# Optimization experiments

Hardware: AMD Instinct MI355X
Metric: run time of the kernel (lower is better)

The kernel has to match this reference:

```python
import jax, jax.numpy as jnp
import numpy as np

B, S, D, C, H, E, K, L = 32, 512, 768, 3072, 1024, 8, 2, 2


def _layernorm(x, g, b, eps=1e-5):
    mu = jnp.mean(x, axis=-1, keepdims=True)
    var = jnp.var(x, axis=-1, keepdims=True)
    return (x - mu) * jax.lax.rsqrt(var + eps) * g + b


def setup_inputs() -> dict:
    key = jax.random.key(0)
    ks = jax.random.split(key, 12)
    s = 0.02
    return {
        "hidden_states": jax.random.normal(ks[0], (B, S, C), jnp.float32),
        "proj_w": jax.random.normal(ks[1], (C, D), jnp.float32) * s,
        "proj_b": jnp.zeros((D,), jnp.float32),
        "ln1_g": jnp.ones((D,), jnp.float32),
        "ln1_b": jnp.zeros((D,), jnp.float32),
        "gate_w": jax.random.normal(ks[2], (D, E), jnp.float32) * s,
        "gate_b": jnp.zeros((E,), jnp.float32),
        "w1": jax.random.normal(ks[3], (E, D, H), jnp.float32) * s,
        "b1": jnp.zeros((E, H), jnp.float32),
        "w2": jax.random.normal(ks[4], (E, H, D), jnp.float32) * s,
        "b2": jnp.zeros((E, D), jnp.float32),
        "ln2_g": jnp.ones((D,), jnp.float32),
        "ln2_b": jnp.zeros((D,), jnp.float32),
        "cls_w": jax.random.normal(ks[5], (D, L), jnp.float32) * s,
        "cls_b": jnp.zeros((L,), jnp.float32),
    }


def reference(hidden_states, proj_w, proj_b, ln1_g, ln1_b, gate_w, gate_b,
              w1, b1, w2, b2, ln2_g, ln2_b, cls_w, cls_b):
    # layer_projection: Linear -> LayerNorm -> GELU (dropout = identity in eval)
    x = jnp.einsum('bsc,cd->bsd', hidden_states, proj_w) + proj_b
    x = _layernorm(x, ln1_g, ln1_b)
    seq_out = jax.nn.gelu(x, approximate=False)  # [B,S,D]

    # Router: gate -> softmax -> top-k -> renormalize
    probs = jax.nn.softmax(seq_out @ gate_w + gate_b, axis=-1)  # [B,S,E]
    top_w, top_i = jax.lax.top_k(probs, K)                      # [B,S,K]
    top_w = top_w / jnp.sum(top_w, axis=-1, keepdims=True)

    # combine[t,e] = sum_k top_w[t,k] * (top_i[t,k]==e)
    combine = jnp.sum(jax.nn.one_hot(top_i, E, dtype=top_w.dtype)
                      * top_w[..., None], axis=-2)              # [B,S,E]

    xt = seq_out.reshape(-1, D)                                 # [T,D]
    ct = combine.reshape(-1, E)                                 # [T,E]
    h = jax.nn.gelu(jnp.einsum('td,edh->eth', xt, w1) + b1[:, None, :],
                    approximate=False)                          # [E,T,H]
    eo = jnp.einsum('eth,ehd->etd', h, w2) + b2[:, None, :]     # [E,T,D]
    moe = jnp.einsum('etd,te->td', eo, ct).reshape(B, S, D)

    moe = _layernorm(moe + seq_out, ln2_g, ln2_b)
    logits = moe @ cls_w + cls_b                                # [B,S,2]
    return logits
```

## Files before the change

kernel.cpp:

```cpp
#include <hip/hip_runtime.h>
#include <hip/hip_bf16.h>

#define T_TOK 16384
#define CDIM 3072
#define DDIM 768
#define HDIM 1024
#define NEXP 8
#define NSLOT 33792
#define MAXTILE 264
#define AMB_CAP 2048
#define AMB2_CAP 256
#define KSPLIT 4
#define NSEG 8

typedef __attribute__((ext_vector_type(8))) short bfrag;
typedef __attribute__((ext_vector_type(4))) float f32x4;
typedef __attribute__((ext_vector_type(4))) float fvec4;

__device__ __forceinline__ unsigned short bf16_rn(float f) {
  union { float f; unsigned u; } v; v.f = f;
  unsigned r = v.u + 0x7fffu + ((v.u >> 16) & 1u);
  return (unsigned short)(r >> 16);
}
__device__ __forceinline__ float bf16_f32(unsigned short h) {
  union { unsigned u; float f; } v; v.u = ((unsigned)h) << 16;
  return v.f;
}
__device__ __forceinline__ float gelu_exact(float x) {
  return 0.5f * x * (1.0f + erff(x * 0.70710678118654752440f));
}
__device__ __forceinline__ void glds16(const void* g, void* l) {
  __builtin_amdgcn_global_load_lds((const __attribute__((address_space(1))) void*)g,
                                   (__attribute__((address_space(3))) void*)l, 16, 0, 0);
}

__global__ void k_init(int* token_list, int* counts, int* cursors, unsigned short* zero_row,
                       int* amb_count, int* amb2_count) {
  int i = blockIdx.x * 256 + threadIdx.x;
  for (int j = i; j < NSLOT; j += 64 * 256) token_list[j] = -1;
  if (i < NEXP) counts[i] = 0;
  if (i < 128) cursors[i] = 0;
  if (i == 0) { *amb_count = 0; *amb2_count = 0; }
  if (i < 1024) zero_row[i] = 0;
}

__global__ void k_cast_tiled(const float* __restrict__ src,
                             unsigned short* __restrict__ dst) {
  __shared__ unsigned short h[128][136];
  int rb = blockIdx.x;
  int cc = blockIdx.y;
  int tid = threadIdx.x;
  const float* in = src + ((size_t)rb * 128) * CDIM + cc * 128;
#pragma unroll
  for (int it = 0; it < 16; ++it) {
    int idx = it * 256 + tid;
    int r = idx >> 5, nv = idx & 31;
    fvec4 v = *(const fvec4*)(in + (size_t)r * CDIM + nv * 4);
    unsigned long long p = (unsigned long long)bf16_rn(v[0]) |
                           ((unsigned long long)bf16_rn(v[1]) << 16) |
                           ((unsigned long long)bf16_rn(v[2]) << 32) |
                           ((unsigned long long)bf16_rn(v[3]) << 48);
    *(unsigned long long*)&h[r][nv * 4] = p;
  }
  __syncthreads();
  unsigned short* ob = dst + ((size_t)rb * 96 + cc * 4) * 4096;
#pragma unroll
  for (int kt = 0; kt < 4; ++kt) {
#pragma unroll
    for (int it = 0; it < 2; ++it) {
      int gg = it * 256 + tid;
      int kg = gg >> 7, r = gg & 127;
      bfrag o = *(const bfrag*)&h[r][kt * 32 + kg * 8];
      *(bfrag*)(ob + ((size_t)kt * 512 + gg) * 8) = o;
    }
  }
}

__global__ void k_transpose_split(const float* __restrict__ src,
                                  unsigned short* __restrict__ dhi,
                                  unsigned short* __restrict__ dlo) {
  __shared__ unsigned short h[128][72], l[128][72];
  int nb2 = blockIdx.x;
  int cb = blockIdx.y;
  int col_blk = nb2 >> 1, nhalf = nb2 & 1;
  int n0 = col_blk * 128 + nhalf * 64;
  int tid = threadIdx.x;
  const float* in = src + (size_t)(cb * 128) * DDIM + n0;
#pragma unroll
  for (int it = 0; it < 8; ++it) {
    int idx = it * 256 + tid;
    int cl = idx >> 4, nv = idx & 15;
    fvec4 v = *(const fvec4*)(in + (size_t)cl * DDIM + nv * 4);
    unsigned long long ph = 0, pl = 0;
#pragma unroll
    for (int e = 0; e < 4; ++e) {
      unsigned short hh = bf16_rn(v[e]);
      unsigned short ll = bf16_rn(v[e] - bf16_f32(hh));
      ph |= (unsigned long long)hh << (16 * e);
      pl |= (unsigned long long)ll << (16 * e);
    }
    *(unsigned long long*)&h[cl][nv * 4] = ph;
    *(unsigned long long*)&l[cl][nv * 4] = pl;
  }
  __syncthreads();
  size_t obase = ((size_t)col_blk * 96 + cb * 4) * 4096;
#pragma unroll
  for (int kt = 0; kt < 4; ++kt) {
    int kg = tid >> 6, rl = tid & 63;
    bfrag oh, ol;
#pragma unroll
    for (int e = 0; e < 8; ++e) {
      int c = kt * 32 + kg * 8 + e;
      oh[e] = (short)h[c][rl];
      ol[e] = (short)l[c][rl];
    }
    size_t gi = obase + ((size_t)kt * 512 + kg * 128 + nhalf * 64 + rl) * 8;
    *(bfrag*)(dhi + gi) = oh;
    *(bfrag*)(dlo + gi) = ol;
  }
}

__global__ void k_transpose_tiled(const float* __restrict__ src0,
                                  unsigned short* __restrict__ dst0, int K, int N) {
  __shared__ unsigned short h[128][72];
  int nb2 = blockIdx.x;
  int cb = blockIdx.y;
  int z = blockIdx.z;
  int col_blk = nb2 >> 1, nhalf = nb2 & 1;
  int n0 = col_blk * 128 + nhalf * 64;
  int tid = threadIdx.x;
  const float* in = src0 + (size_t)z * K * N + (size_t)(cb * 128) * N + n0;
#pragma unroll
  for (int it = 0; it < 8; ++it) {
    int idx = it * 256 + tid;
    int cl = idx >> 4, nv = idx & 15;
    fvec4 v = *(const fvec4*)(in + (size_t)cl * N + nv * 4);
    unsigned long long ph = 0;
#pragma unroll
    for (int e = 0; e < 4; ++e)
      ph |= (unsigned long long)bf16_rn(v[e]) << (16 * e);
    *(unsigned long long*)&h[cl][nv * 4] = ph;
  }
  __syncthreads();
  size_t obase = (size_t)z * K * N + ((size_t)col_blk * (K / 32) + cb * 4) * 4096;
#pragma unroll
  for (int kt = 0; kt < 4; ++kt) {
    int kg = tid >> 6, rl = tid & 63;
    bfrag oh;
#pragma unroll
    for (int e = 0; e < 8; ++e) oh[e] = (short)h[kt * 32 + kg * 8 + e][rl];
    *(bfrag*)(dst0 + obase + ((size_t)kt * 512 + kg * 128 + nhalf * 64 + rl) * 8) = oh;
  }
}

__launch_bounds__(256, 3)
__global__ void k_gemm1(const unsigned short* __restrict__ Atil,
                        const unsigned short* __restrict__ Btil,
                        float* __restrict__ Cout)
{
  __shared__ unsigned short sA[12288], sB[12288];
  int tid = threadIdx.x;
  int lane = tid & 63, wave = tid >> 6;
  int id = blockIdx.x;
  int swz = (id & 7) * 96 + (id >> 3);
  int brow = swz / 6, bcol = swz % 6;
  int row0 = brow * 128, col0 = bcol * 128;
  int wm = wave >> 1, wn = wave & 1;

  f32x4 acc[4][4];
#pragma unroll
  for (int i = 0; i < 4; ++i)
#pragma unroll
    for (int j = 0; j < 4; ++j) acc[i][j] = (f32x4){0.f, 0.f, 0.f, 0.f};

  int rsel = lane & 15, kq = lane >> 4;
  const unsigned short* At = Atil + (size_t)(brow * 96) * 4096;
  const unsigned short* Bt = Btil + (size_t)(bcol * 96) * 4096;

  auto STAGE = [&](int kt, int b) {
    const unsigned short* as = At + (size_t)kt * 4096;
    const unsigned short* bs = Bt + (size_t)kt * 4096;
    int lbase = b * 4096;
#pragma unroll
    for (int pass = 0; pass < 2; ++pass) {
      int g = pass * 256 + tid;
      int li = lbase + (pass * 256 + wave * 64) * 8;
      glds16(as + (size_t)g * 8, &sA[li]);
      glds16(bs + (size_t)g * 8, &sB[li]);
    }
  };

  STAGE(0, 0);
  STAGE(1, 1);
  int b0 = 0;
  for (int kt = 0; kt < 96; ++kt) {
    if (kt < 95) asm volatile("s_waitcnt vmcnt(4)" ::: "memory");
    else         asm volatile("s_waitcnt vmcnt(0)" ::: "memory");
    __builtin_amdgcn_s_barrier();
    if (kt + 2 < 96) {
      int bn = b0 + 2; if (bn >= 3) bn -= 3;
      STAGE(kt + 2, bn);
    }
    int lb = b0 * 4096;
    bfrag af[4], bf[4];
#pragma unroll
    for (int i = 0; i < 4; ++i) {
      af[i] = *(const bfrag*)&sA[lb + (kq * 128 + wm * 64 + i * 16 + rsel) * 8];
      bf[i] = *(const bfrag*)&sB[lb + (kq * 128 + wn * 64 + i * 16 + rsel) * 8];
    }
#pragma unroll
    for (int i = 0; i < 4; ++i)
#pragma unroll
      for (int j = 0; j < 4; ++j)
        acc[i][j] = __builtin_amdgcn_mfma_f32_16x16x32_bf16(af[i], bf[j], acc[i][j], 0, 0, 0);
    b0 = (b0 == 2) ? 0 : b0 + 1;
  }

  int cc = lane & 15, rr = (lane >> 4) * 4;
#pragma unroll
  for (int i = 0; i < 4; ++i)
#pragma unroll
    for (int j = 0; j < 4; ++j)
#pragma unroll
      for (int r = 0; r < 4; ++r) {
        int row = row0 + wm * 64 + i * 16 + rr + r;
        int col = col0 + wn * 64 + j * 16 + cc;
        Cout[(size_t)row * DDIM + col] = acc[i][j][r];
      }
}

__launch_bounds__(256)
__global__ void k_ln_router(const float* __restrict__ xw, const float* __restrict__ proj_b,
                            const float* __restrict__ g1, const float* __restrict__ b1v,
                            const float* __restrict__ gate_w, const float* __restrict__ gate_b,
                            unsigned short* __restrict__ seq_b16,
                            int* __restrict__ top_i, float* __restrict__ top_w,
                            int* __restrict__ amb_list, int* __restrict__ amb_count)
{
  int lane = threadIdx.x & 63;
  int t = blockIdx.x * 4 + (threadIdx.x >> 6);
  const float* xr = xw + (size_t)t * DDIM;
  float x0[12];
  float s = 0.f, s2 = 0.f;
#pragma unroll
  for (int j = 0; j < 12; ++j) {
    int d = lane + 64 * j;
    float v = xr[d] + proj_b[d];
    x0[j] = v; s += v; s2 += v * v;
  }
#pragma unroll
  for (int o = 32; o > 0; o >>= 1) { s += __shfl_xor(s, o, 64); s2 += __shfl_xor(s2, o, 64); }
  float mu = s * (1.f / DDIM);
  float rstd = rsqrtf(s2 * (1.f / DDIM) - mu * mu + 1e-5f);
  float acc8[8];
#pragma unroll
  for (int e = 0; e < 8; ++e) acc8[e] = 0.f;
#pragma unroll
  for (int j = 0; j < 12; ++j) {
    int d = lane + 64 * j;
    float y = (x0[j] - mu) * rstd * g1[d] + b1v[d];
    float ge = gelu_exact(y);
    seq_b16[(size_t)t * DDIM + d] = bf16_rn(ge);
    const float* gw = gate_w + (size_t)d * NEXP;
#pragma unroll
    for (int e = 0; e < 8; ++e) acc8[e] += ge * gw[e];
  }
#pragma unroll
  for (int e = 0; e < 8; ++e)
#pragma unroll
    for (int o = 32; o > 0; o >>= 1) acc8[e] += __shfl_xor(acc8[e], o, 64);
  if (lane == 0) {
    float lg[8];
#pragma unroll
    for (int e = 0; e < 8; ++e) lg[e] = acc8[e] + gate_b[e];
    int i0 = 0;
    for (int e = 1; e < 8; ++e) if (lg[e] > lg[i0]) i0 = e;
    int i1 = (i0 == 0) ? 1 : 0;
    for (int e = 0; e < 8; ++e) if (e != i0 && lg[e] > lg[i1]) i1 = e;
    float l2 = -1e30f;
    for (int e = 0; e < 8; ++e) if (e != i0 && e != i1 && lg[e] > l2) l2 = lg[e];
    if (lg[i1] - l2 < 8e-3f) {
      int p = atomicAdd(amb_count, 1);
      if (p < AMB_CAP) amb_list[p] = t;
    }
    float w0 = 1.f / (1.f + expf(lg[i1] - lg[i0]));
    top_i[t * 2] = i0; top_i[t * 2 + 1] = i1;
    top_w[t * 2] = w0; top_w[t * 2 + 1] = 1.f - w0;
  }
}

__launch_bounds__(256, 2)
__global__ void k_repair(const float* __restrict__ hidden,
                         const unsigned short* __restrict__ BTh,
                         const unsigned short* __restrict__ BTl,
                         const int* __restrict__ amb_list, const int* __restrict__ amb_count,
                         float* __restrict__ xw_fix4)
{
  int n = *amb_count; if (n > AMB_CAP) n = AMB_CAP;
  int by = blockIdx.y;
  if (by * 128 >= n) return;
  int bx = blockIdx.x;
  int z = blockIdx.z;
  int col0 = bx * 128;
  __shared__ unsigned short sAh[8192], sAl[8192], sBh[8192], sBl[8192];
  __shared__ int tk[128];
  int tid = threadIdx.x, lane = tid & 63, wave = tid >> 6;
  if (tid < 128) tk[tid] = (by * 128 + tid < n) ? amb_list[by * 128 + tid] : -1;
  __syncthreads();
  int wm = wave >> 1, wn = wave & 1;
  f32x4 acc[4][4];
#pragma unroll
  for (int i = 0; i < 4; ++i)
#pragma unroll
    for (int j = 0; j < 4; ++j) acc[i][j] = (f32x4){0.f, 0.f, 0.f, 0.f};
  int rsel = lane & 15, kq = lane >> 4;
  int ktbase = z * 24;
  const unsigned short* Bth = BTh + (size_t)(bx * 96) * 4096;
  const unsigned short* Btl = BTl + (size_t)(bx * 96) * 4096;

  auto STAGE = [&](int kt, int b) {
    int k0 = (ktbase + kt) * 32;
    int lb = b * 4096;
    size_t tb = (size_t)(ktbase + kt) * 4096;
#pragma unroll
    for (int pass = 0; pass < 2; ++pass) {
      int g = pass * 256 + tid;
      int kg = g >> 7, r = g & 127;
      int tok = tk[r];
      fvec4 a0 = (fvec4){0.f, 0.f, 0.f, 0.f}, a1 = a0;
      if (tok >= 0) {
        const float* ap = hidden + (size_t)tok * CDIM + k0 + kg * 8;
        a0 = *(const fvec4*)ap;
        a1 = *(const fvec4*)(ap + 4);
      }
      bfrag hv, lv;
#pragma unroll
      for (int u = 0; u < 8; ++u) {
        float v = (u < 4) ? a0[u] : a1[u - 4];
        unsigned short h = bf16_rn(v);
        hv[u] = (short)h;
        lv[u] = (short)bf16_rn(v - bf16_f32(h));
      }
      *(bfrag*)&sAh[lb + (size_t)g * 8] = hv;
      *(bfrag*)&sAl[lb + (size_t)g * 8] = lv;
      int li = lb + (pass * 256 + wave * 64) * 8;
      glds16(Bth + tb + (size_t)g * 8, &sBh[li]);
      glds16(Btl + tb + (size_t)g * 8, &sBl[li]);
    }
  };

  STAGE(0, 0);
  __syncthreads();
  for (int kt = 0; kt < 24; ++kt) {
    int b = kt & 1;
    if (kt + 1 < 24) STAGE(kt + 1, b ^ 1);
    int lb = b * 4096;
    bfrag ah[4], al[4], bh[4], bl[4];
#pragma unroll
    for (int i = 0; i < 4; ++i) {
      int ra = wm * 64 + i * 16 + rsel;
      ah[i] = *(const bfrag*)&sAh[lb + (kq * 128 + ra) * 8];
      al[i] = *(const bfrag*)&sAl[lb + (kq * 128 + ra) * 8];
      int cb = wn * 64 + i * 16 + rsel;
      bh[i] = *(const bfrag*)&sBh[lb + (kq * 128 + cb) * 8];
      bl[i] = *(const bfrag*)&sBl[lb + (kq * 128 + cb) * 8];
    }
#pragma unroll
    for (int i = 0; i < 4; ++i)
#pragma unroll
      for (int j = 0; j < 4; ++j) {
        acc[i][j] = __builtin_amdgcn_mfma_f32_16x16x32_bf16(ah[i], bh[j], acc[i][j], 0, 0, 0);
        acc[i][j] = __builtin_amdgcn_mfma_f32_16x16x32_bf16(ah[i], bl[j], acc[i][j], 0, 0, 0);
        acc[i][j] = __builtin_amdgcn_mfma_f32_16x16x32_bf16(al[i], bh[j], acc[i][j], 0, 0, 0);
      }
    __syncthreads();
  }
  float* dst = xw_fix4 + (size_t)z * AMB_CAP * DDIM;
  int cc = lane & 15, rr = (lane >> 4) * 4;
#pragma unroll
  for (int i = 0; i < 4; ++i)
#pragma unroll
    for (int j = 0; j < 4; ++j)
#pragma unroll
      for (int r = 0; r < 4; ++r) {
        int row = by * 128 + wm * 64 + i * 16 + rr + r;
        int col = col0 + wn * 64 + j * 16 + cc;
        dst[(size_t)row * DDIM + col] = acc[i][j][r];
      }
}

__launch_bounds__(256)
__global__ void k_fix2(const float* __restrict__ xw_fix4, const float* __restrict__ proj_b,
                       const float* __restrict__ g1, const float* __restrict__ b1v,
                       const float* __restrict__ gate_w, const float* __restrict__ gate_b,
                       const int* __restrict__ amb_list, const int* __restrict__ amb_count,
                       int* __restrict__ top_i, float* __restrict__ top_w,
                       int* __restrict__ amb2_list, int* __restrict__ amb2_count)
{
  int n = *amb_count; if (n > AMB_CAP) n = AMB_CAP;
  int lane = threadIdx.x & 63;
  int slot = blockIdx.x * 4 + (threadIdx.x >> 6);
  if (slot >= n) return;
  int t = amb_list[slot];
  const float* p0 = xw_fix4 + (size_t)slot * DDIM;
  const float* p1 = p0 + (size_t)AMB_CAP * DDIM;
  const float* p2 = p1 + (size_t)AMB_CAP * DDIM;
  const float* p3 = p2 + (size_t)AMB_CAP * DDIM;
  float x0[12];
  float s = 0.f, s2 = 0.f;
#pragma unroll
  for (int j = 0; j < 12; ++j) {
    int d = lane + 64 * j;
    float v = ((p0[d] + p1[d]) + (p2[d] + p3[d])) + proj_b[d];
    x0[j] = v; s += v; s2 += v * v;
  }
#pragma unroll
  for (int o = 32; o > 0; o >>= 1) { s += __shfl_xor(s, o, 64); s2 += __shfl_xor(s2, o, 64); }
  float mu = s * (1.f / DDIM);
  float rstd = rsqrtf(s2 * (1.f / DDIM) - mu * mu + 1e-5f);
  float acc8[8];
#pragma unroll
  for (int e = 0; e < 8; ++e) acc8[e] = 0.f;
#pragma unroll
  for (int j = 0; j < 12; ++j) {
    int d = lane + 64 * j;
    float y = (x0[j] - mu) * rstd * g1[d] + b1v[d];
    float ge = gelu_exact(y);
    const float* gw = gate_w + (size_t)d * NEXP;
#pragma unroll
    for (int e = 0; e < 8; ++e) acc8[e] += ge * gw[e];
  }
#pragma unroll
  for (int e = 0; e < 8; ++e)
#pragma unroll
    for (int o = 32; o > 0; o >>= 1) acc8[e] += __shfl_xor(acc8[e], o, 64);
  if (lane == 0) {
    float lg[8];
#pragma unroll
    for (int e = 0; e < 8; ++e) lg[e] = acc8[e] + gate_b[e];
    int i0 = 0;
    for (int e = 1; e < 8; ++e) if (lg[e] > lg[i0]) i0 = e;
    int i1 = (i0 == 0) ? 1 : 0;
    for (int e = 0; e < 8; ++e) if (e != i0 && lg[e] > lg[i1]) i1 = e;
    float l2 = -1e30f;
    for (int e = 0; e < 8; ++e) if (e != i0 && e != i1 && lg[e] > l2) l2 = lg[e];
    if (lg[i1] - l2 < 2e-4f) {
      int p = atomicAdd(amb2_count, 1);
      if (p < AMB2_CAP) amb2_list[p] = t;
    }
    float w0 = 1.f / (1.f + expf(lg[i1] - lg[i0]));
    top_i[t * 2] = i0; top_i[t * 2 + 1] = i1;
    top_w[t * 2] = w0; top_w[t * 2 + 1] = 1.f - w0;
  }
}

__launch_bounds__(256, 1)
__global__ void k_router_fix(const float* __restrict__ hidden, const float* __restrict__ proj_w,
                             const int* __restrict__ amb2_list, const int* __restrict__ amb2_count,
                             double* __restrict__ xpart)
{
  __shared__ float hrow[384];
  int tid = threadIdx.x;
  int seg = blockIdx.y;
  int cbase = seg * 384;
  int n = *amb2_count; if (n > AMB2_CAP) n = AMB2_CAP;
  for (int ii = blockIdx.x; ii < n; ii += gridDim.x) {
    int t = amb2_list[ii];
    __syncthreads();
    if (tid < 96)
      *(fvec4*)&hrow[tid * 4] = *(const fvec4*)(hidden + (size_t)t * CDIM + cbase + tid * 4);
    __syncthreads();
    double p0a = 0.0, p0b = 0.0, p1a = 0.0, p1b = 0.0, p2a = 0.0, p2b = 0.0;
    for (int c0 = 0; c0 < 384; c0 += 16) {
      float w0r[16], w1r[16], w2r[16];
      const float* wp = proj_w + (size_t)(cbase + c0) * DDIM + tid;
#pragma unroll
      for (int u = 0; u < 16; ++u) {
        w0r[u] = wp[u * DDIM];
        w1r[u] = wp[u * DDIM + 256];
        w2r[u] = wp[u * DDIM + 512];
      }
#pragma unroll
      for (int u = 0; u < 16; ++u) {
        double h = (double)hrow[c0 + u];
        if (u & 1) { p0b += h * (double)w0r[u]; p1b += h * (double)w1r[u]; p2b += h * (double)w2r[u]; }
        else       { p0a += h * (double)w0r[u]; p1a += h * (double)w1r[u]; p2a += h * (double)w2r[u]; }
      }
    }
    double* xp = xpart + ((size_t)seg * AMB2_CAP + ii) * DDIM;
    xp[tid] = p0a + p0b;
    xp[tid + 256] = p1a + p1b;
    xp[tid + 512] = p2a + p2b;
  }
}

__launch_bounds__(256)
__global__ void k_fix3(const double* __restrict__ xpart, const float* __restrict__ proj_b,
                       const float* __restrict__ g1, const float* __restrict__ b1v,
                       const float* __restrict__ gate_w, const float* __restrict__ gate_b,
                       const int* __restrict__ amb2_list, const int* __restrict__ amb2_count,
                       int* __restrict__ top_i, float* __restrict__ top_w)
{
  __shared__ double redA[4], redB[4], red8[4][8];
  int n = *amb2_count; if (n > AMB2_CAP) n = AMB2_CAP;
  int ii = blockIdx.x;
  if (ii >= n) return;
  int t = amb2_list[ii];
  int tid = threadIdx.x, lane = tid & 63, wave = tid >> 6;
  double x[3]; double s = 0.0, s2 = 0.0;
#pragma unroll
  for (int j = 0; j < 3; ++j) {
    int d = tid + 256 * j;
    double acc = (double)proj_b[d];
#pragma unroll
    for (int seg = 0; seg < NSEG; ++seg)
      acc += xpart[((size_t)seg * AMB2_CAP + ii) * DDIM + d];
    x[j] = acc; s += acc; s2 += acc * acc;
  }
#pragma unroll
  for (int o = 32; o > 0; o >>= 1) { s += __shfl_down(s, o, 64); s2 += __shfl_down(s2, o, 64); }
  if (lane == 0) { redA[wave] = s; redB[wave] = s2; }
  __syncthreads();
  double mu = (redA[0] + redA[1] + redA[2] + redA[3]) / DDIM;
  double ms = (redB[0] + redB[1] + redB[2] + redB[3]) / DDIM;
  double rstd = 1.0 / sqrt(ms - mu * mu + 1e-5);
  double a8[8];
#pragma unroll
  for (int e = 0; e < 8; ++e) a8[e] = 0.0;
#pragma unroll
  for (int j = 0; j < 3; ++j) {
    int d = tid + 256 * j;
    double y = (x[j] - mu) * rstd * (double)g1[d] + (double)b1v[d];
    double ge = 0.5 * y * (1.0 + erf(y * 0.7071067811865475244));
#pragma unroll
    for (int e = 0; e < 8; ++e) a8[e] += ge * (double)gate_w[(size_t)d * NEXP + e];
  }
#pragma unroll
  for (int e = 0; e < 8; ++e)
#pragma unroll
    for (int o = 32; o > 0; o >>= 1) a8[e] += __shfl_down(a8[e], o, 64);
  if (lane == 0) {
#pragma unroll
    for (int e = 0; e < 8; ++e) red8[wave][e] = a8[e];
  }
  __syncthreads();
  if (tid == 0) {
    double lg[8];
#pragma unroll
    for (int e = 0; e < 8; ++e)
      lg[e] = red8[0][e] + red8[1][e] + red8[2][e] + red8[3][e] + (double)gate_b[e];
    int i0 = 0;
    for (int e = 1; e < 8; ++e) if (lg[e] > lg[i0]) i0 = e;
    int i1 = (i0 == 0) ? 1 : 0;
    for (int e = 0; e < 8; ++e) if (e != i0 && e != i1 && lg[e] > lg[i1]) i1 = e;
    double w0 = 1.0 / (1.0 + exp(lg[i1] - lg[i0]));
    top_i[t * 2] = i0; top_i[t * 2 + 1] = i1;
    top_w[t * 2] = (float)w0; top_w[t * 2 + 1] = (float)(1.0 - w0);
  }
}

__global__ void k_count(const int* __restrict__ top_i, int* __restrict__ counts) {
  __shared__ int h[NEXP];
  int tid = threadIdx.x;
  if (tid < NEXP) h[tid] = 0;
  __syncthreads();
  for (int i = blockIdx.x * 256 + tid; i < 2 * T_TOK; i += 64 * 256)
    atomicAdd(&h[top_i[i]], 1);
  __syncthreads();
  if (tid < NEXP) atomicAdd(&counts[tid], h[tid]);
}

__global__ void k_offsets(const int* __restrict__ counts, int* __restrict__ seg_start,
                          int* __restrict__ padded_total, int* __restrict__ tile_expert) {
  if (threadIdx.x != 0 || blockIdx.x != 0) return;
  int st[NEXP], en[NEXP];
  int s = 0;
  for (int e = 0; e < NEXP; ++e) {
    st[e] = s; seg_start[e] = s;
    s += (counts[e] + 127) & ~127;
    en[e] = s;
  }
  *padded_total = s;
  int nt = s >> 7;
  for (int x = 0; x < nt; ++x) {
    int r = x << 7, e = 0;
    for (int q = 0; q < NEXP; ++q) if (r >= st[q] && r < en[q]) e = q;
    tile_expert[x] = e;
  }
}

__global__ void k_scatter(const int* __restrict__ top_i, const int* __restrict__ seg_start,
                          int* __restrict__ cursors, int* __restrict__ token_list,
                          int* __restrict__ slot_of) {
  __shared__ int lc[NEXP];
  __shared__ int lbase[NEXP];
  int tid = threadIdx.x;
  int t = blockIdx.x * 256 + tid;
  if (tid < NEXP) lc[tid] = 0;
  __syncthreads();
  int e0 = top_i[t * 2], e1 = top_i[t * 2 + 1];
  int o0 = atomicAdd(&lc[e0], 1);
  int o1 = atomicAdd(&lc[e1], 1);
  __syncthreads();
  if (tid < NEXP) lbase[tid] = atomicAdd(&cursors[tid << 4], lc[tid]);
  __syncthreads();
  int p0 = seg_start[e0] + lbase[e0] + o0;
  int p1 = seg_start[e1] + lbase[e1] + o1;
  token_list[p0] = t;
  token_list[p1] = t;
  slot_of[t * 2] = p0;
  slot_of[t * 2 + 1] = p1;
}

__launch_bounds__(256, 4)
__global__ void k_gemm2(const unsigned short* __restrict__ Abase,
                        const unsigned short* __restrict__ w1T,
                        const float* __restrict__ b1,
                        const int* __restrict__ token_list,
                        const int* __restrict__ tile_expert,
                        const int* __restrict__ padded_total,
                        const unsigned short* __restrict__ zero_row,
                        unsigned short* __restrict__ hbuf)
{
  int by = blockIdx.x;
  if (by * 128 >= *padded_total) return;
  int bx = blockIdx.y;
  int e = tile_expert[by];
  __shared__ unsigned short sA[8192], sB[8192];
  __shared__ int tk[128];
  int tid = threadIdx.x, lane = tid & 63, wave = tid >> 6;
  if (tid < 128) tk[tid] = token_list[by * 128 + tid];
  __syncthreads();
  int col0 = bx * 128;
  int wm = wave >> 1, wn = wave & 1;
  f32x4 acc[4][4];
#pragma unroll
  for (int i = 0; i < 4; ++i)
#pragma unroll
    for (int j = 0; j < 4; ++j) acc[i][j] = (f32x4){0.f, 0.f, 0.f, 0.f};
  const unsigned short* Bt = w1T + (size_t)e * HDIM * DDIM + (size_t)bx * (DDIM / 32) * 4096;
  int rsel = lane & 15, kq = lane >> 4;

  auto STAGE = [&](int kt, int b) {
    int k0 = kt * 32;
    int lbase2 = b * 4096;
    size_t tb = (size_t)kt * 4096;
#pragma unroll
    for (int pass = 0; pass < 2; ++pass) {
      int g = pass * 256 + tid;
      int kg = g >> 7, r = g & 127;
      int tok = tk[r];
      const unsigned short* asrc =
          (tok >= 0) ? (Abase + (size_t)tok * DDIM + k0 + kg * 8) : zero_row;
      int li = lbase2 + (pass * 256 + wave * 64) * 8;
      glds16(asrc, &sA[li]);
      glds16(Bt + tb + (size_t)g * 8, &sB[li]);
    }
  };

  STAGE(0, 0);
  __syncthreads();
  for (int kt = 0; kt < 24; ++kt) {
    int b = kt & 1;
    if (kt + 1 < 24) STAGE(kt + 1, b ^ 1);
    int lb = b * 4096;
    bfrag af[4], bf[4];
#pragma unroll
    for (int i = 0; i < 4; ++i) {
      af[i] = *(const bfrag*)&sA[lb + (kq * 128 + wm * 64 + i * 16 + rsel) * 8];
      bf[i] = *(const bfrag*)&sB[lb + (kq * 128 + wn * 64 + i * 16 + rsel) * 8];
    }
#pragma unroll
    for (int i = 0; i < 4; ++i)
#pragma unroll
      for (int j = 0; j < 4; ++j)
        acc[i][j] = __builtin_amdgcn_mfma_f32_16x16x32_bf16(af[i], bf[j], acc[i][j], 0, 0, 0);
    __syncthreads();
  }
  int cc = lane & 15, rr = (lane >> 4) * 4;
#pragma unroll
  for (int i = 0; i < 4; ++i)
#pragma unroll
    for (int j = 0; j < 4; ++j)
#pragma unroll
      for (int r = 0; r < 4; ++r) {
        int row = by * 128 + wm * 64 + i * 16 + rr + r;
        int col = col0 + wn * 64 + j * 16 + cc;
        float x = acc[i][j][r] + b1[(size_t)e * HDIM + col];
        hbuf[(size_t)row * HDIM + col] = bf16_rn(gelu_exact(x));
      }
}

__launch_bounds__(256, 4)
__global__ void k_gemm3(const unsigned short* __restrict__ hbuf,
                        const unsigned short* __restrict__ w2T,
                        const float* __restrict__ b2,
                        const int* __restrict__ tile_expert,
                        const int* __restrict__ padded_total,
                        float* __restrict__ eo)
{
  int by = blockIdx.x;
  if (by * 128 >= *padded_total) return;
  int bx = blockIdx.y;
  int e = tile_expert[by];
  __shared__ unsigned short sA[8192], sB[8192];
  int tid = threadIdx.x, lane = tid & 63, wave = tid >> 6;
  int col0 = bx * 128;
  int wm = wave >> 1, wn = wave & 1;
  f32x4 acc[4][4];
#pragma unroll
  for (int i = 0; i < 4; ++i)
#pragma unroll
    for (int j = 0; j < 4; ++j) acc[i][j] = (f32x4){0.f, 0.f, 0.f, 0.f};
  const unsigned short* Bt = w2T + (size_t)e * DDIM * HDIM + (size_t)bx * (HDIM / 32) * 4096;
  int rsel = lane & 15, kq = lane >> 4;

  auto STAGE = [&](int kt, int b) {
    int k0 = kt * 32;
    int lbase2 = b * 4096;
    size_t tb = (size_t)kt * 4096;
#pragma unroll
    for (int pass = 0; pass < 2; ++pass) {
      int g = pass * 256 + tid;
      int kg = g >> 7, r = g & 127;
      int li = lbase2 + (pass * 256 + wave * 64) * 8;
      glds16(hbuf + (size_t)(by * 128 + r) * HDIM + k0 + kg * 8, &sA[li]);
      glds16(Bt + tb + (size_t)g * 8, &sB[li]);
    }
  };

  STAGE(0, 0);
  __syncthreads();
  for (int kt = 0; kt < 32; ++kt) {
    int b = kt & 1;
    if (kt + 1 < 32) STAGE(kt + 1, b ^ 1);
    int lb = b * 4096;
    bfrag af[4], bf[4];
#pragma unroll
    for (int i = 0; i < 4; ++i) {
      af[i] = *(const bfrag*)&sA[lb + (kq * 128 + wm * 64 + i * 16 + rsel) * 8];
      bf[i] = *(const bfrag*)&sB[lb + (kq * 128 + wn * 64 + i * 16 + rsel) * 8];
    }
#pragma unroll
    for (int i = 0; i < 4; ++i)
#pragma unroll
      for (int j = 0; j < 4; ++j)
        acc[i][j] = __builtin_amdgcn_mfma_f32_16x16x32_bf16(af[i], bf[j], acc[i][j], 0, 0, 0);
    __syncthreads();
  }
  int cc = lane & 15, rr = (lane >> 4) * 4;
#pragma unroll
  for (int i = 0; i < 4; ++i)
#pragma unroll
    for (int j = 0; j < 4; ++j)
#pragma unroll
      for (int r = 0; r < 4; ++r) {
        int row = by * 128 + wm * 64 + i * 16 + rr + r;
        int col = col0 + wn * 64 + j * 16 + cc;
        eo[(size_t)row * DDIM + col] = acc[i][j][r] + b2[(size_t)e * DDIM + col];
      }
}

__launch_bounds__(256)
__global__ void k_combine(const float* __restrict__ eo, const unsigned short* __restrict__ seqb,
                          const int* __restrict__ slot_of, const float* __restrict__ top_w,
                          const float* __restrict__ g2, const float* __restrict__ b2v,
                          const float* __restrict__ cls_w, const float* __restrict__ cls_b,
                          float* __restrict__ out)
{
  int lane = threadIdx.x & 63;
  int t = blockIdx.x * 4 + (threadIdx.x >> 6);
  int s0 = slot_of[t * 2], s1 = slot_of[t * 2 + 1];
  float w0 = top_w[t * 2], w1 = top_w[t * 2 + 1];
  const float* p0 = eo + (size_t)s0 * DDIM;
  const float* p1 = eo + (size_t)s1 * DDIM;
  const unsigned short* sq = seqb + (size_t)t * DDIM;
  float m[12];
  float s = 0.f, s2 = 0.f;
#pragma unroll
  for (int j = 0; j < 12; ++j) {
    int d = lane + 64 * j;
    float v = w0 * p0[d] + w1 * p1[d] + bf16_f32(sq[d]);
    m[j] = v; s += v; s2 += v * v;
  }
#pragma unroll
  for (int o = 32; o > 0; o >>= 1) { s += __shfl_xor(s, o, 64); s2 += __shfl_xor(s2, o, 64); }
  float mu = s * (1.f / DDIM);
  float rstd = rsqrtf(s2 * (1.f / DDIM) - mu * mu + 1e-5f);
  float l0 = 0.f, l1 = 0.f;
#pragma unroll
  for (int j = 0; j < 12; ++j) {
    int d = lane + 64 * j;
    float y = (m[j] - mu) * rstd * g2[d] + b2v[d];
    l0 += y * cls_w[d * 2];
    l1 += y * cls_w[d * 2 + 1];
  }
#pragma unroll
  for (int o = 32; o > 0; o >>= 1) { l0 += __shfl_xor(l0, o, 64); l1 += __shfl_xor(l1, o, 64); }
  if (lane == 0) {
    out[(size_t)t * 2] = l0 + cls_b[0];
    out[(size_t)t * 2 + 1] = l1 + cls_b[1];
  }
}

extern "C" void kernel_launch(void* const* d_in, const int* in_sizes, int n_in,
                              void* d_out, int out_size, void* d_ws, size_t ws_size,
                              hipStream_t stream) {
  const float* hidden = (const float*)d_in[0];
  const float* proj_w = (const float*)d_in[1];
  const float* proj_b = (const float*)d_in[2];
  const float* ln1_g  = (const float*)d_in[3];
  const float* ln1_b  = (const float*)d_in[4];
  const float* gate_w = (const float*)d_in[5];
  const float* gate_b = (const float*)d_in[6];
  const float* w1     = (const float*)d_in[7];
  const float* b1     = (const float*)d_in[8];
  const float* w2     = (const float*)d_in[9];
  const float* b2     = (const float*)d_in[10];
  const float* ln2_g  = (const float*)d_in[11];
  const float* ln2_b  = (const float*)d_in[12];
  const float* cls_w  = (const float*)d_in[13];
  const float* cls_b  = (const float*)d_in[14];
  float* out = (float*)d_out;

  char* base = (char*)d_ws;
  size_t off = 0;
  auto alloc = [&](size_t b) -> void* {
    void* p = base + off;
    off += (b + 255) & ~(size_t)255;
    return p;
  };
  unsigned short* pwT_hi = (unsigned short*)alloc((size_t)DDIM * CDIM * 2);
  unsigned short* pwT_lo = (unsigned short*)alloc((size_t)DDIM * CDIM * 2);
  unsigned short* w1T    = (unsigned short*)alloc((size_t)NEXP * HDIM * DDIM * 2);
  unsigned short* w2T    = (unsigned short*)alloc((size_t)NEXP * DDIM * HDIM * 2);
  float* xw              = (float*)alloc((size_t)T_TOK * DDIM * 4);
  float* xw_fix4         = (float*)alloc((size_t)KSPLIT * AMB_CAP * DDIM * 4);
  double* xpart          = (double*)alloc((size_t)NSEG * AMB2_CAP * DDIM * 8);
  unsigned short* seqb   = (unsigned short*)alloc((size_t)T_TOK * DDIM * 2);
  int* top_i             = (int*)alloc((size_t)T_TOK * 2 * 4);
  float* top_w           = (float*)alloc((size_t)T_TOK * 2 * 4);
  int* slot_of           = (int*)alloc((size_t)T_TOK * 2 * 4);
  int* amb_list          = (int*)alloc((size_t)AMB_CAP * 4);
  int* amb2_list         = (int*)alloc((size_t)AMB2_CAP * 4);
  int* token_list        = (int*)alloc((size_t)NSLOT * 4);
  int* counts            = (int*)alloc(256);
  int* cursors           = (int*)alloc(512);
  int* seg_start         = (int*)alloc(256);
  int* padded_total      = (int*)alloc(256);
  int* tile_expert       = (int*)alloc((size_t)MAXTILE * 4);
  unsigned short* zero_row = (unsigned short*)alloc(2048);
  int* amb_count         = (int*)alloc(256);
  int* amb2_count        = (int*)alloc(256);
  size_t poolBytes = 2 * (size_t)T_TOK * CDIM * 2;
  char* pool = (char*)alloc(poolBytes);
  unsigned short* Ahi = (unsigned short*)pool;
  size_t poff = 0;
  auto palloc = [&](size_t b) -> void* {
    void* p = pool + poff;
    poff += (b + 255) & ~(size_t)255;
    return p;
  };
  unsigned short* hbuf   = (unsigned short*)palloc((size_t)NSLOT * HDIM * 2);
  float* eo              = (float*)palloc((size_t)NSLOT * DDIM * 4);
  (void)ws_size; (void)in_sizes; (void)n_in; (void)out_size;

  k_init<<<64, 256, 0, stream>>>(token_list, counts, cursors, zero_row, amb_count, amb2_count);
  k_cast_tiled<<<dim3(128, 24), 256, 0, stream>>>(hidden, Ahi);
  k_transpose_split<<<dim3(12, 24), 256, 0, stream>>>(proj_w, pwT_hi, pwT_lo);
  k_transpose_tiled<<<dim3(16, 6, 8), 256, 0, stream>>>(w1, w1T, DDIM, HDIM);
  k_transpose_tiled<<<dim3(12, 8, 8), 256, 0, stream>>>(w2, w2T, HDIM, DDIM);
  k_gemm1<<<768, 256, 0, stream>>>(Ahi, pwT_hi, xw);
  k_ln_router<<<T_TOK / 4, 256, 0, stream>>>(xw, proj_b, ln1_g, ln1_b, gate_w, gate_b,
                                             seqb, top_i, top_w, amb_list, amb_count);
  k_repair<<<dim3(6, AMB_CAP / 128, KSPLIT), 256, 0, stream>>>(hidden, pwT_hi, pwT_lo,
                                                               amb_list, amb_count, xw_fix4);
  k_fix2<<<AMB_CAP / 4, 256, 0, stream>>>(xw_fix4, proj_b, ln1_g, ln1_b, gate_w, gate_b,
                                          amb_list, amb_count, top_i, top_w,
                                          amb2_list, amb2_count);
  k_router_fix<<<dim3(64, NSEG), 256, 0, stream>>>(hidden, proj_w, amb2_list, amb2_count, xpart);
  k_fix3<<<AMB2_CAP, 256, 0, stream>>>(xpart, proj_b, ln1_g, ln1_b, gate_w, gate_b,
                                       amb2_list, amb2_count, top_i, top_w);
  k_count<<<64, 256, 0, stream>>>(top_i, counts);
  k_offsets<<<1, 64, 0, stream>>>(counts, seg_start, padded_total, tile_expert);
  k_scatter<<<64, 256, 0, stream>>>(top_i, seg_start, cursors, token_list, slot_of);
  k_gemm2<<<dim3(MAXTILE, 8), 256, 0, stream>>>(seqb, w1T, b1, token_list, tile_expert,
                                                padded_total, zero_row, hbuf);
  k_gemm3<<<dim3(MAXTILE, 6), 256, 0, stream>>>(hbuf, w2T, b2, tile_expert, padded_total, eo);
  k_combine<<<T_TOK / 4, 256, 0, stream>>>(eo, seqb, slot_of, top_w, ln2_g, ln2_b,
                                           cls_w, cls_b, out);
}
```

Baseline: 643.9 us.

## Pre-gather expert tokens into tile-contiguous layout for MoE GEMMs

Adds a gather kernel that copies routed token rows into a per-tile, k-blocked contiguous buffer, so the first expert GEMM streams its A operand with linear loads instead of per-row indirect gathers. The first GEMM now writes its GELU output directly in the same tiled layout, so the second GEMM also reads A linearly. This is meant to cut scattered, poorly coalesced global loads in both GEMM staging loops. In exchange it adds an extra kernel launch and a copy of the gathered activations, and the first GEMM's epilogue stores become more scattered.

```diff
diff --git a/kernel.cpp b/kernel.cpp
--- a/kernel.cpp
+++ b/kernel.cpp
@@ -612,25 +612,56 @@
   slot_of[t * 2 + 1] = p1;
 }
 
+__global__ void k_gather(const unsigned short* __restrict__ seqb,
+                         const int* __restrict__ token_list,
+                         const int* __restrict__ padded_total,
+                         unsigned short* __restrict__ seqgT) {
+  int sb = blockIdx.x;
+  if (sb * 128 >= *padded_total) return;
+  int cc = blockIdx.y;
+  __shared__ unsigned short h[128][136];
+  __shared__ int tk[128];
+  int tid = threadIdx.x;
+  if (tid < 128) tk[tid] = token_list[sb * 128 + tid];
+  __syncthreads();
+#pragma unroll
+  for (int it = 0; it < 8; ++it) {
+    int idx = it * 256 + tid;
+    int r = idx >> 4, nv = idx & 15;
+    int tok = tk[r];
+    bfrag v = (bfrag){0, 0, 0, 0, 0, 0, 0, 0};
+    if (tok >= 0)
+      v = *(const bfrag*)(seqb + (size_t)tok * DDIM + cc * 128 + nv * 8);
+    *(bfrag*)&h[r][nv * 8] = v;
+  }
+  __syncthreads();
+  unsigned short* ob = seqgT + ((size_t)sb * 24 + cc * 4) * 4096;
+#pragma unroll
+  for (int kt = 0; kt < 4; ++kt) {
+#pragma unroll
+    for (int it = 0; it < 2; ++it) {
+      int gg = it * 256 + tid;
+      int kg = gg >> 7, r = gg & 127;
+      bfrag o = *(const bfrag*)&h[r][kt * 32 + kg * 8];
+      *(bfrag*)(ob + ((size_t)kt * 512 + gg) * 8) = o;
+    }
+  }
+}
+
 __launch_bounds__(256, 4)
-__global__ void k_gemm2(const unsigned short* __restrict__ Abase,
+__global__ void k_gemm2(const unsigned short* __restrict__ seqgT,
                         const unsigned short* __restrict__ w1T,
                         const float* __restrict__ b1,
-                        const int* __restrict__ token_list,
                         const int* __restrict__ tile_expert,
                         const int* __restrict__ padded_total,
-                        const unsigned short* __restrict__ zero_row,
-                        unsigned short* __restrict__ hbuf)
+                        unsigned short* __restrict__ hbufT)
 {
   int by = blockIdx.x;
   if (by * 128 >= *padded_total) return;
   int bx = blockIdx.y;
   int e = tile_expert[by];
   __shared__ unsigned short sA[8192], sB[8192];
-  __shared__ int tk[128];
   int tid = threadIdx.x, lane = tid & 63, wave = tid >> 6;
-  if (tid < 128) tk[tid] = token_list[by * 128 + tid];
-  __syncthreads();
   int col0 = bx * 128;
   int wm = wave >> 1, wn = wave & 1;
   f32x4 acc[4][4];
@@ -638,22 +669,18 @@
   for (int i = 0; i < 4; ++i)
 #pragma unroll
     for (int j = 0; j < 4; ++j) acc[i][j] = (f32x4){0.f, 0.f, 0.f, 0.f};
-  const unsigned short* Bt = w1T + (size_t)e * HDIM * DDIM + (size_t)bx * (DDIM / 32) * 4096;
+  const unsigned short* At = seqgT + (size_t)by * 24 * 4096;
+  const unsigned short* Bt = w1T + (size_t)e * HDIM * DDIM + (size_t)bx * 24 * 4096;
   int rsel = lane & 15, kq = lane >> 4;
 
   auto STAGE = [&](int kt, int b) {
-    int k0 = kt * 32;
     int lbase2 = b * 4096;
     size_t tb = (size_t)kt * 4096;
 #pragma unroll
     for (int pass = 0; pass < 2; ++pass) {
       int g = pass * 256 + tid;
-      int kg = g >> 7, r = g & 127;
-      int tok = tk[r];
-      const unsigned short* asrc =
-          (tok >= 0) ? (Abase + (size_t)tok * DDIM + k0 + kg * 8) : zero_row;
       int li = lbase2 + (pass * 256 + wave * 64) * 8;
-      glds16(asrc, &sA[li]);
+      glds16(At + tb + (size_t)g * 8, &sA[li]);
       glds16(Bt + tb + (size_t)g * 8, &sB[li]);
     }
   };
@@ -684,15 +711,17 @@
     for (int j = 0; j < 4; ++j)
 #pragma unroll
       for (int r = 0; r < 4; ++r) {
-        int row = by * 128 + wm * 64 + i * 16 + rr + r;
+        int lr = wm * 64 + i * 16 + rr + r;
         int col = col0 + wn * 64 + j * 16 + cc;
         float x = acc[i][j][r] + b1[(size_t)e * HDIM + col];
-        hbuf[(size_t)row * HDIM + col] = bf16_rn(gelu_exact(x));
+        size_t tile = (size_t)by * 32 + (col >> 5);
+        int g = ((col >> 3) & 3) * 128 + lr;
+        hbufT[tile * 4096 + g * 8 + (col & 7)] = bf16_rn(gelu_exact(x));
       }
 }
 
 __launch_bounds__(256, 4)
-__global__ void k_gemm3(const unsigned short* __restrict__ hbuf,
+__global__ void k_gemm3(const unsigned short* __restrict__ hbufT,
                         const unsigned short* __restrict__ w2T,
                         const float* __restrict__ b2,
                         const int* __restrict__ tile_expert,
@@ -712,19 +741,18 @@
   for (int i = 0; i < 4; ++i)
 #pragma unroll
     for (int j = 0; j < 4; ++j) acc[i][j] = (f32x4){0.f, 0.f, 0.f, 0.f};
-  const unsigned short* Bt = w2T + (size_t)e * DDIM * HDIM + (size_t)bx * (HDIM / 32) * 4096;
+  const unsigned short* At = hbufT + (size_t)by * 32 * 4096;
+  const unsigned short* Bt = w2T + (size_t)e * DDIM * HDIM + (size_t)bx * 32 * 4096;
   int rsel = lane & 15, kq = lane >> 4;
 
   auto STAGE = [&](int kt, int b) {
-    int k0 = kt * 32;
     int lbase2 = b * 4096;
     size_t tb = (size_t)kt * 4096;
 #pragma unroll
     for (int pass = 0; pass < 2; ++pass) {
       int g = pass * 256 + tid;
-      int kg = g >> 7, r = g & 127;
       int li = lbase2 + (pass * 256 + wave * 64) * 8;
-      glds16(hbuf + (size_t)(by * 128 + r) * HDIM + k0 + kg * 8, &sA[li]);
+      glds16(At + tb + (size_t)g * 8, &sA[li]);
       glds16(Bt + tb + (size_t)g * 8, &sB[li]);
     }
   };
@@ -838,6 +866,7 @@
   float* xw_fix4         = (float*)alloc((size_t)KSPLIT * AMB_CAP * DDIM * 4);
   double* xpart          = (double*)alloc((size_t)NSEG * AMB2_CAP * DDIM * 8);
   unsigned short* seqb   = (unsigned short*)alloc((size_t)T_TOK * DDIM * 2);
+  unsigned short* seqgT  = (unsigned short*)alloc((size_t)MAXTILE * 24 * 4096 * 2);
   int* top_i             = (int*)alloc((size_t)T_TOK * 2 * 4);
   float* top_w           = (float*)alloc((size_t)T_TOK * 2 * 4);
   int* slot_of           = (int*)alloc((size_t)T_TOK * 2 * 4);
@@ -861,7 +890,7 @@
     poff += (b + 255) & ~(size_t)255;
     return p;
   };
-  unsigned short* hbuf   = (unsigned short*)palloc((size_t)NSLOT * HDIM * 2);
+  unsigned short* hbufT  = (unsigned short*)palloc((size_t)MAXTILE * 32 * 4096 * 2);
   float* eo              = (float*)palloc((size_t)NSLOT * DDIM * 4);
   (void)ws_size; (void)in_sizes; (void)n_in; (void)out_size;
 
@@ -884,9 +913,10 @@
   k_count<<<64, 256, 0, stream>>>(top_i, counts);
   k_offsets<<<1, 64, 0, stream>>>(counts, seg_start, padded_total, tile_expert);
   k_scatter<<<64, 256, 0, stream>>>(top_i, seg_start, cursors, token_list, slot_of);
-  k_gemm2<<<dim3(MAXTILE, 8), 256, 0, stream>>>(seqb, w1T, b1, token_list, tile_expert,
-                                                padded_total, zero_row, hbuf);
-  k_gemm3<<<dim3(MAXTILE, 6), 256, 0, stream>>>(hbuf, w2T, b2, tile_expert, padded_total, eo);
+  k_gather<<<dim3(MAXTILE, 6), 256, 0, stream>>>(seqb, token_list, padded_total, seqgT);
+  k_gemm2<<<dim3(MAXTILE, 8), 256, 0, stream>>>(seqgT, w1T, b1, tile_expert,
+                                                padded_total, hbufT);
+  k_gemm3<<<dim3(MAXTILE, 6), 256, 0, stream>>>(hbufT, w2T, b2, tile_expert, padded_total, eo);
   k_combine<<<T_TOK / 4, 256, 0, stream>>>(eo, seqb, slot_of, top_w, ln2_g, ln2_b,
                                            cls_w, cls_b, out);
 }
```

New measurement: 631.7 us. About the same (-1.9%).
